# Kernel optimization log

Hardware: AMD Instinct MI355X
Metric: run time of the kernel (lower is better)

The kernel has to match this reference:

```python
import jax, jax.numpy as jnp
import numpy as np

DIM = 1024
HEADS = 16
HEAD_DIM = DIM // HEADS
SCALE = HEAD_DIM ** -0.5


def setup_inputs() -> dict:
    key = jax.random.key(0)
    k1, k2, k3, k4 = jax.random.split(key, 4)
    x = jax.random.normal(k1, (4, 2048, DIM), dtype=jnp.float32)
    # nn.Linear weights stored as [out, in]; qkv_bias=False so no proj_in bias
    w_qkv = jax.random.normal(k2, (3 * DIM, DIM), dtype=jnp.float32) * (DIM ** -0.5)
    w_out = jax.random.normal(k3, (DIM, DIM), dtype=jnp.float32) * (DIM ** -0.5)
    b_out = jax.random.normal(k4, (DIM,), dtype=jnp.float32) * 0.01
    return {"x": x, "w_qkv": w_qkv, "w_out": w_out, "b_out": b_out}


def reference(x, w_qkv, w_out, b_out):
    bs, ns, _ = x.shape
    qkv = jnp.einsum("bsd,ed->bse", x, w_qkv)              # [b, s, 3*dim]
    qkv = qkv.reshape(bs, ns, 3, HEADS, HEAD_DIM)
    qkv = jnp.transpose(qkv, (2, 0, 3, 1, 4))               # [3, b, h, s, hd]
    q, k, v = qkv[0], qkv[1], qkv[2]
    attn = jnp.einsum("bhqd,bhkd->bhqk", q, k) * SCALE      # [b, h, s, s]
    attn = jax.nn.softmax(attn, axis=-1)
    out = jnp.einsum("bhqk,bhkd->bhqd", attn, v)            # [b, h, s, hd]
    out = jnp.transpose(out, (0, 2, 1, 3)).reshape(bs, ns, HEADS * HEAD_DIM)
    return jnp.einsum("bsd,ed->bse", out, w_out) + b_out
```

## Files before the change

kernel.cpp:

```cpp
#include <hip/hip_runtime.h>

#define DIM 1024
#define SEQ 2048

typedef unsigned short ushort_t;
typedef unsigned int u32;
typedef __attribute__((ext_vector_type(8))) short short8;
typedef __attribute__((ext_vector_type(8))) unsigned short ushort8;
typedef __attribute__((ext_vector_type(4))) float f32x4;
typedef __attribute__((ext_vector_type(16))) float f32x16;

__device__ __forceinline__ ushort_t f2bf(float x) {
    u32 u = __float_as_uint(x);
    u32 r = (u + 0x7fffu + ((u >> 16) & 1u)) >> 16;
    return (ushort_t)r;
}

__device__ __forceinline__ u32 cvtpk(float lo, float hi) {
    u32 r;
    asm("v_cvt_pk_bf16_f32 %0, %1, %2" : "=v"(r) : "v"(lo), "v"(hi));
    return r;
}

__device__ __forceinline__ void gload16(const void* g, void* l) {
    __builtin_amdgcn_global_load_lds(
        (const __attribute__((address_space(1))) u32*)g,
        (__attribute__((address_space(3))) u32*)l, 16, 0, 0);
}

__device__ __forceinline__ int swz8(int row, int col) {
    return row * 64 + ((((col >> 3) ^ (row & 7)) << 3) | (col & 7));
}

__global__ __launch_bounds__(256) void cvt_bf16(const float* __restrict__ in,
                                                ushort_t* __restrict__ out, int n8) {
    for (int i = blockIdx.x * blockDim.x + threadIdx.x; i < n8; i += gridDim.x * blockDim.x) {
        const float4 a = ((const float4*)in)[2 * i];
        const float4 b = ((const float4*)in)[2 * i + 1];
        ushort8 o;
        o[0] = f2bf(a.x); o[1] = f2bf(a.y); o[2] = f2bf(a.z); o[3] = f2bf(a.w);
        o[4] = f2bf(b.x); o[5] = f2bf(b.y); o[6] = f2bf(b.z); o[7] = f2bf(b.w);
        ((ushort8*)out)[i] = o;
    }
}

template <int EPI>
__global__ __launch_bounds__(256) void gemm_bt(const ushort_t* __restrict__ A,
                                               const ushort_t* __restrict__ B,
                                               const float* __restrict__ bias,
                                               ushort_t* __restrict__ outb,
                                               ushort_t* __restrict__ voutb,
                                               float* __restrict__ outf) {
    __shared__ __align__(16) ushort_t As[128 * 64];
    __shared__ __align__(16) ushort_t Bs[128 * 64];
    const int t = threadIdx.x;
    const int m0 = blockIdx.y * 128, n0 = blockIdx.x * 128;
    const int w = t >> 6, lane = t & 63, k15 = lane & 15, g = lane >> 4;
    const int wm = (w >> 1) * 64, wn = (w & 1) * 64;
    const int srow = t >> 3, scol = (t & 7) * 8;

    f32x4 acc[4][4] = {};

    for (int k0 = 0; k0 < 1024; k0 += 64) {
        __syncthreads();
        #pragma unroll
        for (int i = 0; i < 4; ++i) {
            gload16(&A[(size_t)(m0 + i * 32 + srow) * 1024 + k0 + scol],
                    ((char*)As) + i * 4096 + t * 16);
            gload16(&B[(size_t)(n0 + i * 32 + srow) * 1024 + k0 + scol],
                    ((char*)Bs) + i * 4096 + t * 16);
        }
        __syncthreads();
        #pragma unroll
        for (int ks = 0; ks < 2; ++ks) {
            short8 af[4], bf[4];
            #pragma unroll
            for (int i = 0; i < 4; ++i) {
                af[i] = *(const short8*)&As[(wm + i * 16 + k15) * 64 + ks * 32 + g * 8];
                bf[i] = *(const short8*)&Bs[(wn + i * 16 + k15) * 64 + ks * 32 + g * 8];
            }
            #pragma unroll
            for (int mi = 0; mi < 4; ++mi)
                #pragma unroll
                for (int ni = 0; ni < 4; ++ni)
                    acc[mi][ni] = __builtin_amdgcn_mfma_f32_16x16x32_bf16(
                        af[mi], bf[ni], acc[mi][ni], 0, 0, 0);
        }
    }

    if (EPI == 0) {
        #pragma unroll
        for (int mi = 0; mi < 4; ++mi) {
            const int mbase = m0 + wm + mi * 16 + g * 4;
            const int b = mbase >> 11, s0 = mbase & 2047;
            #pragma unroll
            for (int ni = 0; ni < 4; ++ni) {
                const int e = n0 + wn + ni * 16 + k15;
                const int qi = e >> 10, h = (e >> 6) & 15, hd = e & 63;
                const int bh = b * 16 + h;
                if (qi == 2) {
                    const u32 lo = cvtpk(acc[mi][ni][0], acc[mi][ni][1]);
                    const u32 hi = cvtpk(acc[mi][ni][2], acc[mi][ni][3]);
                    *(uint2*)&voutb[((size_t)bh * 64 + hd) * SEQ + s0] = make_uint2(lo, hi);
                } else {
                    const float scl = (qi == 0) ? 0.180336880f : 1.0f;
                    #pragma unroll
                    for (int r = 0; r < 4; ++r)
                        outb[((size_t)(qi * 64 + bh) * SEQ + s0 + r) * 64 + hd] =
                            f2bf(acc[mi][ni][r] * scl);
                }
            }
        }
    } else {
        #pragma unroll
        for (int mi = 0; mi < 4; ++mi) {
            #pragma unroll
            for (int r = 0; r < 4; ++r) {
                const size_t m = m0 + wm + mi * 16 + g * 4 + r;
                #pragma unroll
                for (int ni = 0; ni < 4; ++ni) {
                    const int e = n0 + wn + ni * 16 + k15;
                    outf[m * 1024 + e] = acc[mi][ni][r] + bias[e];
                }
            }
        }
    }
}

__global__ __launch_bounds__(256, 4) void attn_mfma(const ushort_t* __restrict__ qk,
                                                    const ushort_t* __restrict__ vt,
                                                    ushort_t* __restrict__ aout) {
    __shared__ __align__(16) ushort_t Ks[2][64 * 64];
    __shared__ __align__(16) ushort_t Vs[2][64 * 64];

    const int t = threadIdx.x, w = t >> 6, lane = t & 63;
    const int l31 = lane & 31, hi = lane >> 5;

    const int bid = blockIdx.x + (blockIdx.y << 4);
    const int j   = bid >> 3;
    const int bh  = ((bid & 7) << 3) + (j >> 4);
    const int q0  = (j & 15) * 128;

    const ushort_t* Qp = qk + (size_t)bh * SEQ * 64;
    const ushort_t* Kp = qk + (size_t)(64 + bh) * SEQ * 64;
    const ushort_t* Vp = vt + (size_t)bh * 64 * SEQ;
    const int wq = q0 + w * 32 + l31;

    const int srow = t >> 3;
    const int scb8 = ((t & 7) ^ (srow & 7)) * 8;

    const ushort_t* kpA = Kp + (size_t)srow * 64 + scb8;
    const ushort_t* vpA = Vp + (size_t)srow * SEQ + scb8;

    short8 qf[4];
    #pragma unroll
    for (int kc = 0; kc < 4; ++kc)
        qf[kc] = *(const short8*)&Qp[(size_t)wq * 64 + kc * 16 + hi * 8];

    gload16(kpA,            ((char*)Ks) + t * 16);
    gload16(kpA + 32 * 64,  ((char*)Ks) + 4096 + t * 16);
    gload16(vpA,            ((char*)Vs) + t * 16);
    gload16(vpA + 32 * SEQ, ((char*)Vs) + 4096 + t * 16);
    kpA += 64 * 64; vpA += 64;
    __syncthreads();

    f32x16 o2[2] = {};
    float li = 0.f;
    int cur = 0;

    for (int kt = 0; kt < SEQ / 64; ++kt) {
        if (kt + 1 < SEQ / 64) {
            char* dstK = ((char*)Ks) + (cur ^ 1) * 8192 + t * 16;
            char* dstV = ((char*)Vs) + (cur ^ 1) * 8192 + t * 16;
            gload16(kpA,            dstK);
            gload16(kpA + 32 * 64,  dstK + 4096);
            gload16(vpA,            dstV);
            gload16(vpA + 32 * SEQ, dstV + 4096);
            kpA += 64 * 64; vpA += 64;
        }

        f32x16 s32[2] = {};
        __builtin_amdgcn_s_setprio(1);
        #pragma unroll
        for (int kt2 = 0; kt2 < 2; ++kt2) {
            #pragma unroll
            for (int kc = 0; kc < 4; ++kc) {
                const short8 kf = *(const short8*)&Ks[cur][swz8(kt2 * 32 + l31, kc * 16 + hi * 8)];
                s32[kt2] = __builtin_amdgcn_mfma_f32_32x32x16_bf16(
                    kf, qf[kc], s32[kt2], 0, 0, 0);
            }
        }
        __builtin_amdgcn_s_setprio(0);

        {
            float t0 = 0.f, t1 = 0.f, t2 = 0.f, t3 = 0.f;
            #pragma unroll
            for (int kt2 = 0; kt2 < 2; ++kt2) {
                #pragma unroll
                for (int r = 0; r < 16; r += 4) {
                    const float e0 = __builtin_amdgcn_exp2f(s32[kt2][r + 0]);
                    const float e1 = __builtin_amdgcn_exp2f(s32[kt2][r + 1]);
                    const float e2 = __builtin_amdgcn_exp2f(s32[kt2][r + 2]);
                    const float e3 = __builtin_amdgcn_exp2f(s32[kt2][r + 3]);
                    s32[kt2][r + 0] = e0; s32[kt2][r + 1] = e1;
                    s32[kt2][r + 2] = e2; s32[kt2][r + 3] = e3;
                    t0 += e0; t1 += e1; t2 += e2; t3 += e3;
                }
            }
            float rs = (t0 + t1) + (t2 + t3);
            rs += __shfl_xor(rs, 32);
            li += rs;
        }

        uint4 pb[4];
        #pragma unroll
        for (int ks2 = 0; ks2 < 4; ++ks2) {
            const int r0 = (ks2 & 1) * 8;
            const int sv = ks2 >> 1;
            u32 pA = cvtpk(s32[sv][r0 + 0], s32[sv][r0 + 1]);
            u32 pB = cvtpk(s32[sv][r0 + 2], s32[sv][r0 + 3]);
            u32 pC = cvtpk(s32[sv][r0 + 4], s32[sv][r0 + 5]);
            u32 pD = cvtpk(s32[sv][r0 + 6], s32[sv][r0 + 7]);
            asm volatile("v_permlane32_swap_b32 %0, %1" : "+v"(pA), "+v"(pC));
            asm volatile("v_permlane32_swap_b32 %0, %1" : "+v"(pB), "+v"(pD));
            pb[ks2] = make_uint4(pA, pB, pC, pD);
        }

        __builtin_amdgcn_s_setprio(1);
        #pragma unroll
        for (int dt = 0; dt < 2; ++dt) {
            #pragma unroll
            for (int ks2 = 0; ks2 < 4; ++ks2) {
                const short8 vf = *(const short8*)&Vs[cur][swz8(dt * 32 + l31, ks2 * 16 + hi * 8)];
                o2[dt] = __builtin_amdgcn_mfma_f32_32x32x16_bf16(
                    vf, *(const short8*)&pb[ks2], o2[dt], 0, 0, 0);
            }
        }
        __builtin_amdgcn_s_setprio(0);

        __syncthreads();
        cur ^= 1;
    }

    const int b = bh >> 4, h = bh & 15;
    const float inv = 1.0f / li;
    const size_t base = ((size_t)b * SEQ + wq) * DIM + h * 64;
    #pragma unroll
    for (int dt = 0; dt < 2; ++dt) {
        #pragma unroll
        for (int rq = 0; rq < 4; ++rq) {
            const u32 lo = cvtpk(o2[dt][4 * rq + 0] * inv, o2[dt][4 * rq + 1] * inv);
            const u32 hg = cvtpk(o2[dt][4 * rq + 2] * inv, o2[dt][4 * rq + 3] * inv);
            *(uint2*)&aout[base + dt * 32 + rq * 8 + hi * 4] = make_uint2(lo, hg);
        }
    }
}

extern "C" void kernel_launch(void* const* d_in, const int* in_sizes, int n_in,
                              void* d_out, int out_size, void* d_ws, size_t ws_size,
                              hipStream_t stream) {
    const float* x     = (const float*)d_in[0];
    const float* w_qkv = (const float*)d_in[1];
    const float* w_out = (const float*)d_in[2];
    const float* b_out = (const float*)d_in[3];
    float* out = (float*)d_out;

    char* ws = (char*)d_ws;
    ushort_t* xb    = (ushort_t*)ws;
    ushort_t* wqkvb = (ushort_t*)(ws + (size_t)16 * 1024 * 1024);
    ushort_t* woutb = (ushort_t*)(ws + (size_t)22 * 1024 * 1024);
    ushort_t* qkb   = (ushort_t*)(ws + (size_t)24 * 1024 * 1024);
    ushort_t* vtb   = (ushort_t*)(ws + (size_t)56 * 1024 * 1024);
    ushort_t* aob   = (ushort_t*)(ws + (size_t)72 * 1024 * 1024);

    cvt_bf16<<<1024, 256, 0, stream>>>(x,     xb,    8192 * 1024 / 8);
    cvt_bf16<<<512,  256, 0, stream>>>(w_qkv, wqkvb, 3072 * 1024 / 8);
    cvt_bf16<<<256,  256, 0, stream>>>(w_out, woutb, 1024 * 1024 / 8);

    gemm_bt<0><<<dim3(24, 64), 256, 0, stream>>>(xb, wqkvb, nullptr, qkb, vtb, nullptr);
    attn_mfma<<<dim3(16, 64), 256, 0, stream>>>(qkb, vtb, aob);
    gemm_bt<1><<<dim3(8, 64), 256, 0, stream>>>(aob, woutb, b_out, nullptr, nullptr, out);
}
```

Before: 213.3 us.

## Process two 32-row query tiles per wave to double K/V reuse in attention

```diff
diff --git a/kernel.cpp b/kernel.cpp
--- a/kernel.cpp
+++ b/kernel.cpp
@@ -127,7 +127,7 @@
     }
 }
 
-__global__ __launch_bounds__(256, 4) void attn_mfma(const ushort_t* __restrict__ qk,
+__global__ __launch_bounds__(256, 2) void attn_mfma(const ushort_t* __restrict__ qk,
                                                     const ushort_t* __restrict__ vt,
                                                     ushort_t* __restrict__ aout) {
     __shared__ __align__(16) ushort_t Ks[2][64 * 64];
@@ -136,15 +136,16 @@
     const int t = threadIdx.x, w = t >> 6, lane = t & 63;
     const int l31 = lane & 31, hi = lane >> 5;
 
-    const int bid = blockIdx.x + (blockIdx.y << 4);
+    const int bid = blockIdx.x;
     const int j   = bid >> 3;
-    const int bh  = ((bid & 7) << 3) + (j >> 4);
-    const int q0  = (j & 15) * 128;
+    const int bh  = ((bid & 7) << 3) + (j >> 3);
+    const int q0  = (j & 7) * 256;
 
     const ushort_t* Qp = qk + (size_t)bh * SEQ * 64;
     const ushort_t* Kp = qk + (size_t)(64 + bh) * SEQ * 64;
     const ushort_t* Vp = vt + (size_t)bh * 64 * SEQ;
-    const int wq = q0 + w * 32 + l31;
+    const int wqA = q0 + w * 64 + l31;
+    const int wqB = wqA + 32;
 
     const int srow = t >> 3;
     const int scb8 = ((t & 7) ^ (srow & 7)) * 8;
@@ -152,10 +153,12 @@
     const ushort_t* kpA = Kp + (size_t)srow * 64 + scb8;
     const ushort_t* vpA = Vp + (size_t)srow * SEQ + scb8;
 
-    short8 qf[4];
+    short8 qfA[4], qfB[4];
     #pragma unroll
-    for (int kc = 0; kc < 4; ++kc)
-        qf[kc] = *(const short8*)&Qp[(size_t)wq * 64 + kc * 16 + hi * 8];
+    for (int kc = 0; kc < 4; ++kc) {
+        qfA[kc] = *(const short8*)&Qp[(size_t)wqA * 64 + kc * 16 + hi * 8];
+        qfB[kc] = *(const short8*)&Qp[(size_t)wqB * 64 + kc * 16 + hi * 8];
+    }
 
     gload16(kpA,            ((char*)Ks) + t * 16);
     gload16(kpA + 32 * 64,  ((char*)Ks) + 4096 + t * 16);
@@ -164,8 +167,8 @@
     kpA += 64 * 64; vpA += 64;
     __syncthreads();
 
-    f32x16 o2[2] = {};
-    float li = 0.f;
+    f32x16 oA[2] = {}, oB[2] = {};
+    float liA = 0.f, liB = 0.f;
     int cur = 0;
 
     for (int kt = 0; kt < SEQ / 64; ++kt) {
@@ -179,51 +182,79 @@
             kpA += 64 * 64; vpA += 64;
         }
 
-        f32x16 s32[2] = {};
+        f32x16 sA[2] = {}, sB[2] = {};
         __builtin_amdgcn_s_setprio(1);
         #pragma unroll
         for (int kt2 = 0; kt2 < 2; ++kt2) {
             #pragma unroll
             for (int kc = 0; kc < 4; ++kc) {
                 const short8 kf = *(const short8*)&Ks[cur][swz8(kt2 * 32 + l31, kc * 16 + hi * 8)];
-                s32[kt2] = __builtin_amdgcn_mfma_f32_32x32x16_bf16(
-                    kf, qf[kc], s32[kt2], 0, 0, 0);
+                sA[kt2] = __builtin_amdgcn_mfma_f32_32x32x16_bf16(kf, qfA[kc], sA[kt2], 0, 0, 0);
+                sB[kt2] = __builtin_amdgcn_mfma_f32_32x32x16_bf16(kf, qfB[kc], sB[kt2], 0, 0, 0);
             }
         }
         __builtin_amdgcn_s_setprio(0);
 
+        uint4 pbA[4], pbB[4];
         {
             float t0 = 0.f, t1 = 0.f, t2 = 0.f, t3 = 0.f;
             #pragma unroll
-            for (int kt2 = 0; kt2 < 2; ++kt2) {
+            for (int kt2 = 0; kt2 < 2; ++kt2)
                 #pragma unroll
                 for (int r = 0; r < 16; r += 4) {
-                    const float e0 = __builtin_amdgcn_exp2f(s32[kt2][r + 0]);
-                    const float e1 = __builtin_amdgcn_exp2f(s32[kt2][r + 1]);
-                    const float e2 = __builtin_amdgcn_exp2f(s32[kt2][r + 2]);
-                    const float e3 = __builtin_amdgcn_exp2f(s32[kt2][r + 3]);
-                    s32[kt2][r + 0] = e0; s32[kt2][r + 1] = e1;
-                    s32[kt2][r + 2] = e2; s32[kt2][r + 3] = e3;
+                    const float e0 = __builtin_amdgcn_exp2f(sA[kt2][r + 0]);
+                    const float e1 = __builtin_amdgcn_exp2f(sA[kt2][r + 1]);
+                    const float e2 = __builtin_amdgcn_exp2f(sA[kt2][r + 2]);
+                    const float e3 = __builtin_amdgcn_exp2f(sA[kt2][r + 3]);
+                    sA[kt2][r + 0] = e0; sA[kt2][r + 1] = e1;
+                    sA[kt2][r + 2] = e2; sA[kt2][r + 3] = e3;
                     t0 += e0; t1 += e1; t2 += e2; t3 += e3;
                 }
-            }
             float rs = (t0 + t1) + (t2 + t3);
             rs += __shfl_xor(rs, 32);
-            li += rs;
-        }
-
-        uint4 pb[4];
-        #pragma unroll
-        for (int ks2 = 0; ks2 < 4; ++ks2) {
-            const int r0 = (ks2 & 1) * 8;
-            const int sv = ks2 >> 1;
-            u32 pA = cvtpk(s32[sv][r0 + 0], s32[sv][r0 + 1]);
-            u32 pB = cvtpk(s32[sv][r0 + 2], s32[sv][r0 + 3]);
-            u32 pC = cvtpk(s32[sv][r0 + 4], s32[sv][r0 + 5]);
-            u32 pD = cvtpk(s32[sv][r0 + 6], s32[sv][r0 + 7]);
-            asm volatile("v_permlane32_swap_b32 %0, %1" : "+v"(pA), "+v"(pC));
-            asm volatile("v_permlane32_swap_b32 %0, %1" : "+v"(pB), "+v"(pD));
-            pb[ks2] = make_uint4(pA, pB, pC, pD);
+            liA += rs;
+            #pragma unroll
+            for (int ks2 = 0; ks2 < 4; ++ks2) {
+                const int r0 = (ks2 & 1) * 8;
+                const int sv = ks2 >> 1;
+                u32 pA = cvtpk(sA[sv][r0 + 0], sA[sv][r0 + 1]);
+                u32 pB = cvtpk(sA[sv][r0 + 2], sA[sv][r0 + 3]);
+                u32 pC = cvtpk(sA[sv][r0 + 4], sA[sv][r0 + 5]);
+                u32 pD = cvtpk(sA[sv][r0 + 6], sA[sv][r0 + 7]);
+                asm volatile("v_permlane32_swap_b32 %0, %1" : "+v"(pA), "+v"(pC));
+                asm volatile("v_permlane32_swap_b32 %0, %1" : "+v"(pB), "+v"(pD));
+                pbA[ks2] = make_uint4(pA, pB, pC, pD);
+            }
+        }
+        {
+            float t0 = 0.f, t1 = 0.f, t2 = 0.f, t3 = 0.f;
+            #pragma unroll
+            for (int kt2 = 0; kt2 < 2; ++kt2)
+                #pragma unroll
+                for (int r = 0; r < 16; r += 4) {
+                    const float e0 = __builtin_amdgcn_exp2f(sB[kt2][r + 0]);
+                    const float e1 = __builtin_amdgcn_exp2f(sB[kt2][r + 1]);
+                    const float e2 = __builtin_amdgcn_exp2f(sB[kt2][r + 2]);
+                    const float e3 = __builtin_amdgcn_exp2f(sB[kt2][r + 3]);
+                    sB[kt2][r + 0] = e0; sB[kt2][r + 1] = e1;
+                    sB[kt2][r + 2] = e2; sB[kt2][r + 3] = e3;
+                    t0 += e0; t1 += e1; t2 += e2; t3 += e3;
+                }
+            float rs = (t0 + t1) + (t2 + t3);
+            rs += __shfl_xor(rs, 32);
+            liB += rs;
+            #pragma unroll
+            for (int ks2 = 0; ks2 < 4; ++ks2) {
+                const int r0 = (ks2 & 1) * 8;
+                const int sv = ks2 >> 1;
+                u32 pA = cvtpk(sB[sv][r0 + 0], sB[sv][r0 + 1]);
+                u32 pB = cvtpk(sB[sv][r0 + 2], sB[sv][r0 + 3]);
+                u32 pC = cvtpk(sB[sv][r0 + 4], sB[sv][r0 + 5]);
+                u32 pD = cvtpk(sB[sv][r0 + 6], sB[sv][r0 + 7]);
+                asm volatile("v_permlane32_swap_b32 %0, %1" : "+v"(pA), "+v"(pC));
+                asm volatile("v_permlane32_swap_b32 %0, %1" : "+v"(pB), "+v"(pD));
+                pbB[ks2] = make_uint4(pA, pB, pC, pD);
+            }
         }
 
         __builtin_amdgcn_s_setprio(1);
@@ -232,8 +263,10 @@
             #pragma unroll
             for (int ks2 = 0; ks2 < 4; ++ks2) {
                 const short8 vf = *(const short8*)&Vs[cur][swz8(dt * 32 + l31, ks2 * 16 + hi * 8)];
-                o2[dt] = __builtin_amdgcn_mfma_f32_32x32x16_bf16(
-                    vf, *(const short8*)&pb[ks2], o2[dt], 0, 0, 0);
+                oA[dt] = __builtin_amdgcn_mfma_f32_32x32x16_bf16(
+                    vf, *(const short8*)&pbA[ks2], oA[dt], 0, 0, 0);
+                oB[dt] = __builtin_amdgcn_mfma_f32_32x32x16_bf16(
+                    vf, *(const short8*)&pbB[ks2], oB[dt], 0, 0, 0);
             }
         }
         __builtin_amdgcn_s_setprio(0);
@@ -243,16 +276,29 @@
     }
 
     const int b = bh >> 4, h = bh & 15;
-    const float inv = 1.0f / li;
-    const size_t base = ((size_t)b * SEQ + wq) * DIM + h * 64;
-    #pragma unroll
-    for (int dt = 0; dt < 2; ++dt) {
-        #pragma unroll
-        for (int rq = 0; rq < 4; ++rq) {
-            const u32 lo = cvtpk(o2[dt][4 * rq + 0] * inv, o2[dt][4 * rq + 1] * inv);
-            const u32 hg = cvtpk(o2[dt][4 * rq + 2] * inv, o2[dt][4 * rq + 3] * inv);
-            *(uint2*)&aout[base + dt * 32 + rq * 8 + hi * 4] = make_uint2(lo, hg);
-        }
+    {
+        const float inv = 1.0f / liA;
+        const size_t base = ((size_t)b * SEQ + wqA) * DIM + h * 64;
+        #pragma unroll
+        for (int dt = 0; dt < 2; ++dt)
+            #pragma unroll
+            for (int rq = 0; rq < 4; ++rq) {
+                const u32 lo = cvtpk(oA[dt][4 * rq + 0] * inv, oA[dt][4 * rq + 1] * inv);
+                const u32 hg = cvtpk(oA[dt][4 * rq + 2] * inv, oA[dt][4 * rq + 3] * inv);
+                *(uint2*)&aout[base + dt * 32 + rq * 8 + hi * 4] = make_uint2(lo, hg);
+            }
+    }
+    {
+        const float inv = 1.0f / liB;
+        const size_t base = ((size_t)b * SEQ + wqB) * DIM + h * 64;
+        #pragma unroll
+        for (int dt = 0; dt < 2; ++dt)
+            #pragma unroll
+            for (int rq = 0; rq < 4; ++rq) {
+                const u32 lo = cvtpk(oB[dt][4 * rq + 0] * inv, oB[dt][4 * rq + 1] * inv);
+                const u32 hg = cvtpk(oB[dt][4 * rq + 2] * inv, oB[dt][4 * rq + 3] * inv);
+                *(uint2*)&aout[base + dt * 32 + rq * 8 + hi * 4] = make_uint2(lo, hg);
+            }
     }
 }
 
@@ -278,6 +324,6 @@
     cvt_bf16<<<256,  256, 0, stream>>>(w_out, woutb, 1024 * 1024 / 8);
 
     gemm_bt<0><<<dim3(24, 64), 256, 0, stream>>>(xb, wqkvb, nullptr, qkb, vtb, nullptr);
-    attn_mfma<<<dim3(16, 64), 256, 0, stream>>>(qkb, vtb, aob);
+    attn_mfma<<<512, 256, 0, stream>>>(qkb, vtb, aob);
     gemm_bt<1><<<dim3(8, 64), 256, 0, stream>>>(aob, woutb, b_out, nullptr, nullptr, out);
 }
```

Measured after the change: 202.9 us, median of 3. 1.05x faster.
